# Optimization experiments

Hardware: AMD Instinct MI355X
Metric: run time of the kernel (lower is better)

## Reference

```python
import jax, jax.numpy as jnp
import numpy as np

BN_EPS = 1e-5


def setup_inputs() -> dict:
    key = jax.random.key(0)
    ks = jax.random.split(key, 5)
    b, c, h, w = 4, 128, 64, 64
    x = jax.random.normal(ks[0], (b, c, h, w), dtype=jnp.float32)
    # conv1x1 c -> 2c (fan-in scaled)
    w_inp = jax.random.normal(ks[1], (2 * c, c), dtype=jnp.float32) / np.sqrt(c)
    b_inp = jax.random.normal(ks[2], (2 * c,), dtype=jnp.float32) * 0.01
    bn_gamma = jnp.ones((2 * c,), dtype=jnp.float32)
    bn_beta = jnp.zeros((2 * c,), dtype=jnp.float32)
    bn_mean = jnp.zeros((2 * c,), dtype=jnp.float32)
    bn_var = jnp.ones((2 * c,), dtype=jnp.float32)
    w_out = jax.random.normal(ks[3], (c, c), dtype=jnp.float32) / np.sqrt(c)
    b_out = jax.random.normal(ks[4], (c,), dtype=jnp.float32) * 0.01
    return {
        "x": x, "w_inp": w_inp, "b_inp": b_inp,
        "bn_gamma": bn_gamma, "bn_beta": bn_beta,
        "bn_mean": bn_mean, "bn_var": bn_var,
        "w_out": w_out, "b_out": b_out,
    }


def reference(x, w_inp, b_inp, bn_gamma, bn_beta, bn_mean, bn_var, w_out, b_out):
    b, c, h, w = x.shape
    scale = c ** (-0.5)
    # project_inp: conv1x1 (c -> 2c) + BatchNorm2d (eval mode, running stats)
    t = jnp.einsum('bchw,oc->bohw', x, w_inp) + b_inp[None, :, None, None]
    bn_scale = bn_gamma * jax.lax.rsqrt(bn_var + BN_EPS)
    t = t * bn_scale[None, :, None, None] + (bn_beta - bn_mean * bn_scale)[None, :, None, None]
    # split qv along channels, flatten spatial to tokens: [b, N, c], N = h*w
    q = t[:, :c].reshape(b, c, h * w).transpose(0, 2, 1)
    v = t[:, c:].reshape(b, c, h * w).transpose(0, 2, 1)
    # self-similarity attention on q: [b, N, N]
    atn = jax.nn.softmax(jnp.einsum('bnc,bmc->bnm', q, q) * scale, axis=-1)
    y = jnp.einsum('bnm,bmc->bnc', atn, v)  # [b, N, c]
    y = y.transpose(0, 2, 1).reshape(b, c, h, w)
    # project_out: conv1x1 c -> c
    y = jnp.einsum('bchw,oc->bohw', y, w_out) + b_out[None, :, None, None]
    return (y, atn)
```

## Files before the change

kernel.cpp:

```cpp
#include <hip/hip_runtime.h>
#include <stdint.h>
#include <math.h>

#define C_DIM 128
#define N_TOK 4096
#define NB 4
#define LOG2E 1.4426950408889634f

typedef __attribute__((ext_vector_type(8))) short bf16x8;
typedef __attribute__((ext_vector_type(4))) float f32x4;

__device__ __forceinline__ unsigned short f2bf(float f) {
  unsigned u = __builtin_bit_cast(unsigned, f);
  unsigned r = (u + 0x7FFFu + ((u >> 16) & 1u)) >> 16;
  return (unsigned short)r;
}
__device__ __forceinline__ float bf2f(unsigned short h) {
  return __builtin_bit_cast(float, ((unsigned)h) << 16);
}
__device__ __forceinline__ void gload_lds16(const void* g, void* l) {
  __builtin_amdgcn_global_load_lds((const __attribute__((address_space(1))) void*)g,
                                   (__attribute__((address_space(3))) void*)l,
                                   16, 0, 0);
}

__global__ __launch_bounds__(256) void proj_in_kernel(
    const float* __restrict__ x, const float* __restrict__ w_inp,
    const float* __restrict__ b_inp, const float* __restrict__ gamma,
    const float* __restrict__ beta, const float* __restrict__ mean,
    const float* __restrict__ var,
    unsigned short* __restrict__ q, unsigned short* __restrict__ vT) {
  __shared__ char smem[35840];
  unsigned short* xh = (unsigned short*)smem;
  unsigned short* xl = (unsigned short*)(smem + 17408);

  const int tid = threadIdx.x;
  const int b = blockIdx.x >> 6;
  const int n0 = (blockIdx.x & 63) << 6;
  const int lane = tid & 63;
  const int wave = tid >> 6;
  const int l15 = lane & 15, lg = lane >> 4;

  {
    const int c = tid >> 1;
    const int j0 = (tid & 1) * 32;
    const float* src = x + ((size_t)b * C_DIM + c) * N_TOK + n0 + j0;
#pragma unroll
    for (int j = 0; j < 32; j += 4) {
      float4 v4 = *(const float4*)(src + j);
#pragma unroll
      for (int e = 0; e < 4; e++) {
        float f = (&v4.x)[e];
        unsigned short hi = f2bf(f);
        unsigned short lo = f2bf(f - bf2f(hi));
        int n = j0 + j + e;
        xh[n * 136 + c] = hi;
        xl[n * 136 + c] = lo;
      }
    }
  }
  __syncthreads();

  f32x4 acc[4][4];
#pragma unroll
  for (int i = 0; i < 4; i++)
#pragma unroll
    for (int j = 0; j < 4; j++) acc[i][j] = {0.f, 0.f, 0.f, 0.f};

#pragma unroll
  for (int ks = 0; ks < 4; ks++) {
    bf16x8 ah[4], al[4];
#pragma unroll
    for (int ot = 0; ot < 4; ot++) {
      const int o = wave * 64 + ot * 16 + l15;
      const float* wp = w_inp + o * C_DIM + ks * 32 + lg * 8;
      float4 w0 = *(const float4*)wp;
      float4 w1 = *(const float4*)(wp + 4);
#pragma unroll
      for (int e = 0; e < 8; e++) {
        float f = (e < 4) ? (&w0.x)[e] : (&w1.x)[e - 4];
        unsigned short hi = f2bf(f);
        ah[ot][e] = (short)hi;
        al[ot][e] = (short)f2bf(f - bf2f(hi));
      }
    }
#pragma unroll
    for (int nt = 0; nt < 4; nt++) {
      const int off = (nt * 16 + l15) * 136 + ks * 32 + lg * 8;
      bf16x8 bh = *(const bf16x8*)(xh + off);
      bf16x8 bl = *(const bf16x8*)(xl + off);
#pragma unroll
      for (int ot = 0; ot < 4; ot++) {
        acc[ot][nt] = __builtin_amdgcn_mfma_f32_16x16x32_bf16(ah[ot], bh, acc[ot][nt], 0, 0, 0);
        acc[ot][nt] = __builtin_amdgcn_mfma_f32_16x16x32_bf16(ah[ot], bl, acc[ot][nt], 0, 0, 0);
        acc[ot][nt] = __builtin_amdgcn_mfma_f32_16x16x32_bf16(al[ot], bh, acc[ot][nt], 0, 0, 0);
      }
    }
  }
  __syncthreads();

  unsigned short* qT = (unsigned short*)smem;
  unsigned short* vTl = (unsigned short*)(smem + 17408);

#pragma unroll
  for (int ot = 0; ot < 4; ot++) {
#pragma unroll
    for (int r = 0; r < 4; r++) {
      const int o = wave * 64 + ot * 16 + lg * 4 + r;
      float A = gamma[o] * rsqrtf(var[o] + 1e-5f);
      float Bo = beta[o] + (b_inp[o] - mean[o]) * A;
#pragma unroll
      for (int nt = 0; nt < 4; nt++) {
        float val = acc[ot][nt][r] * A + Bo;
        unsigned short hv = f2bf(val);
        int n = nt * 16 + l15;
        if (wave < 2) {
          qT[n * 136 + o] = hv;
        } else {
          vTl[(o - 128) * 72 + n] = hv;
        }
      }
    }
  }
  __syncthreads();
  {
    int j = tid >> 2, c0 = (tid & 3) * 32;
    unsigned short* dst = q + ((size_t)b * N_TOK + n0 + j) * C_DIM + c0;
    const unsigned short* s = qT + j * 136 + c0;
#pragma unroll
    for (int i = 0; i < 32; i += 8) *(bf16x8*)(dst + i) = *(const bf16x8*)(s + i);
  }
  {
    int c = tid >> 1, h = (tid & 1) * 32;
    unsigned short* dst = vT + ((size_t)b * C_DIM + c) * N_TOK + n0 + h;
    const unsigned short* s = vTl + c * 72 + h;
#pragma unroll
    for (int i = 0; i < 32; i += 8) *(bf16x8*)(dst + i) = *(const bf16x8*)(s + i);
  }
}

__global__ __launch_bounds__(256) void attn_kernel(
    const unsigned short* __restrict__ q, const unsigned short* __restrict__ vT,
    const float* __restrict__ w_out, const float* __restrict__ b_out,
    float* __restrict__ yout, float* __restrict__ atn) {
  __shared__ char smem[71168];

  const int tid = threadIdx.x;
  const int lane = tid & 63;
  const int wave = tid >> 6;
  const int rg = wave >> 1;
  const int kh = wave & 1;
  const int l15 = lane & 15, lg = lane >> 4, l7 = lane & 7;
  const int b = blockIdx.x >> 7;
  const int q0 = (blockIdx.x & 127) << 5;
  const int row0 = q0 + rg * 16;

  const unsigned short* qb = q + (size_t)b * N_TOK * C_DIM;
  const unsigned short* vb = vT + (size_t)b * C_DIM * N_TOK;

  bf16x8 qf[4];
#pragma unroll
  for (int ks = 0; ks < 4; ks++)
    qf[ks] = *(const bf16x8*)(qb + (size_t)(row0 + l15) * C_DIM + ks * 32 + lg * 8);

  int koff[4];
#pragma unroll
  for (int ks = 0; ks < 4; ks++) koff[ks] = (ks * 64 + lg * 16) ^ (l7 * 16);
  const int koff2 = (kh * 64 + lg * 16) ^ (l7 * 16);
  const int krow = l15 * 256;
  const int vrow = l15 * 128;

  auto stageK = [&](int kt, int buf) {
    char* base = smem + buf * 16384;
#pragma unroll
    for (int i = 0; i < 4; i++) {
      int lin = i * 256 + tid;
      int key = lin >> 4;
      int c = ((lin & 15) * 8) ^ ((key & 7) * 8);
      gload_lds16(qb + (size_t)(kt * 64 + key) * C_DIM + c, base + lin * 16);
    }
  };
  auto stageV = [&](int kt, int buf) {
    char* base = smem + 32768 + buf * 16384;
#pragma unroll
    for (int i = 0; i < 4; i++) {
      int lin = i * 256 + tid;
      int c = lin >> 3;
      int key = ((lin & 7) * 8) ^ ((c & 7) * 8);
      gload_lds16(vb + (size_t)c * N_TOK + kt * 64 + key, base + lin * 16);
    }
  };

  const float scale = 0.08838834764831845f;
  float m[4], l[4], invl[4];
#pragma unroll
  for (int r = 0; r < 4; r++) { m[r] = -1e30f; l[r] = 0.f; }

  stageK(0, 0);
  __syncthreads();
  for (int kt = 0; kt < 64; kt++) {
    if (kt + 1 < 64) stageK(kt + 1, (kt + 1) & 1);
    const char* kb = smem + (kt & 1) * 16384;
    float s_all[2][4];
#pragma unroll
    for (int nt16 = 0; nt16 < 2; nt16++) {
      const int nt = kh * 2 + nt16;
      f32x4 acc = {0.f, 0.f, 0.f, 0.f};
#pragma unroll
      for (int ks = 0; ks < 4; ks++) {
        bf16x8 bk = *(const bf16x8*)(kb + nt * 4096 + krow + koff[ks]);
        acc = __builtin_amdgcn_mfma_f32_16x16x32_bf16(qf[ks], bk, acc, 0, 0, 0);
      }
#pragma unroll
      for (int r = 0; r < 4; r++) s_all[nt16][r] = acc[r] * scale;
    }
#pragma unroll
    for (int r = 0; r < 4; r++) {
      float mx = fmaxf(s_all[0][r], s_all[1][r]);
      mx = fmaxf(mx, __shfl_xor(mx, 1));
      mx = fmaxf(mx, __shfl_xor(mx, 2));
      mx = fmaxf(mx, __shfl_xor(mx, 4));
      mx = fmaxf(mx, __shfl_xor(mx, 8));
      float mn = fmaxf(m[r], mx);
      float sum = exp2f((s_all[0][r] - mn) * LOG2E) + exp2f((s_all[1][r] - mn) * LOG2E);
      sum += __shfl_xor(sum, 1);
      sum += __shfl_xor(sum, 2);
      sum += __shfl_xor(sum, 4);
      sum += __shfl_xor(sum, 8);
      l[r] = l[r] * exp2f((m[r] - mn) * LOG2E) + sum;
      m[r] = mn;
    }
    __syncthreads();
  }

  float* statsL = (float*)(smem + 70656);
  if (l15 == 0) {
#pragma unroll
    for (int r = 0; r < 4; r++) {
      float* p = statsL + (((kh * 2 + rg) * 16) + lg * 4 + r) * 2;
      p[0] = m[r];
      p[1] = l[r];
    }
  }
  __syncthreads();
#pragma unroll
  for (int r = 0; r < 4; r++) {
    const int row = lg * 4 + r;
    const float* p0 = statsL + ((rg * 16) + row) * 2;
    const float* p1 = statsL + (((2 + rg) * 16) + row) * 2;
    float m0 = p0[0], l0 = p0[1], m1 = p1[0], l1 = p1[1];
    float M = fmaxf(m0, m1);
    float L = l0 * exp2f((m0 - M) * LOG2E) + l1 * exp2f((m1 - M) * LOG2E);
    m[r] = M;
    invl[r] = 1.0f / L;
  }

  f32x4 yacc[8];
#pragma unroll
  for (int ct = 0; ct < 8; ct++) yacc[ct] = {0.f, 0.f, 0.f, 0.f};

  stageK(0, 0);
  stageV(0, 0);
  __syncthreads();
  unsigned short* pb = (unsigned short*)(smem + 65536 + wave * 1280);
  float* atnb = atn + ((size_t)b * N_TOK + row0) * N_TOK;

  for (int kt = 0; kt < 64; kt++) {
    if (kt + 1 < 64) { stageK(kt + 1, (kt + 1) & 1); stageV(kt + 1, (kt + 1) & 1); }
    const char* kb = smem + (kt & 1) * 16384;
    const char* vbf = smem + 32768 + (kt & 1) * 16384;
#pragma unroll
    for (int nt16 = 0; nt16 < 2; nt16++) {
      const int nt = kh * 2 + nt16;
      f32x4 acc = {0.f, 0.f, 0.f, 0.f};
#pragma unroll
      for (int ks = 0; ks < 4; ks++) {
        bf16x8 bk = *(const bf16x8*)(kb + nt * 4096 + krow + koff[ks]);
        acc = __builtin_amdgcn_mfma_f32_16x16x32_bf16(qf[ks], bk, acc, 0, 0, 0);
      }
#pragma unroll
      for (int r = 0; r < 4; r++) {
        float p = exp2f((acc[r] * scale - m[r]) * LOG2E) * invl[r];
        atnb[(size_t)(lg * 4 + r) * N_TOK + kt * 64 + kh * 32 + nt16 * 16 + l15] = p;
        pb[(lg * 4 + r) * 40 + nt16 * 16 + l15] = (unsigned short)f2bf(p);
      }
    }
    {
      bf16x8 ap = *(const bf16x8*)(pb + l15 * 40 + lg * 8);
#pragma unroll
      for (int ct = 0; ct < 8; ct++) {
        bf16x8 bv = *(const bf16x8*)(vbf + ct * 2048 + vrow + koff2);
        yacc[ct] = __builtin_amdgcn_mfma_f32_16x16x32_bf16(ap, bv, yacc[ct], 0, 0, 0);
      }
    }
    __syncthreads();
  }

  float* ymergeF = (float*)(smem + 32768);
  if (kh) {
#pragma unroll
    for (int ct = 0; ct < 8; ct++)
#pragma unroll
      for (int r = 0; r < 4; r++)
        ymergeF[(rg * 16 + lg * 4 + r) * 136 + ct * 16 + l15] = yacc[ct][r];
  }
  __syncthreads();
  if (!kh) {
#pragma unroll
    for (int ct = 0; ct < 8; ct++)
#pragma unroll
      for (int r = 0; r < 4; r++)
        yacc[ct][r] += ymergeF[(rg * 16 + lg * 4 + r) * 136 + ct * 16 + l15];

    unsigned short* yl = (unsigned short*)(smem + rg * 16384);
    float* ol = (float*)(smem + rg * 16384 + 4608);
#pragma unroll
    for (int ct = 0; ct < 8; ct++)
#pragma unroll
      for (int r = 0; r < 4; r++)
        yl[(lg * 4 + r) * 136 + ct * 16 + l15] = f2bf(yacc[ct][r]);

    bf16x8 af[4];
#pragma unroll
    for (int ks = 0; ks < 4; ks++)
      af[ks] = *(const bf16x8*)(yl + l15 * 136 + ks * 32 + lg * 8);

#pragma unroll
    for (int cot = 0; cot < 8; cot++) {
      f32x4 oacc = {0.f, 0.f, 0.f, 0.f};
#pragma unroll
      for (int ks = 0; ks < 4; ks++) {
        const float* wp = w_out + (cot * 16 + l15) * C_DIM + ks * 32 + lg * 8;
        float4 w0 = *(const float4*)wp;
        float4 w1 = *(const float4*)(wp + 4);
        bf16x8 bw;
#pragma unroll
        for (int e = 0; e < 8; e++) bw[e] = (short)f2bf((e < 4) ? (&w0.x)[e] : (&w1.x)[e - 4]);
        oacc = __builtin_amdgcn_mfma_f32_16x16x32_bf16(af[ks], bw, oacc, 0, 0, 0);
      }
      float bo = b_out[cot * 16 + l15];
#pragma unroll
      for (int r = 0; r < 4; r++) ol[(cot * 16 + l15) * 20 + lg * 4 + r] = oacc[r] + bo;
    }
#pragma unroll
    for (int i = 0; i < 2; i++) {
      int co = i * 64 + lane;
      float* dst = yout + ((size_t)b * C_DIM + co) * N_TOK + row0;
      const float* s = ol + co * 20;
#pragma unroll
      for (int jj = 0; jj < 16; jj += 4) *(float4*)(dst + jj) = *(const float4*)(s + jj);
    }
  }
}

extern "C" void kernel_launch(void* const* d_in, const int* in_sizes, int n_in,
                              void* d_out, int out_size, void* d_ws, size_t ws_size,
                              hipStream_t stream) {
  const float* x = (const float*)d_in[0];
  const float* w_inp = (const float*)d_in[1];
  const float* b_inp = (const float*)d_in[2];
  const float* gamma = (const float*)d_in[3];
  const float* beta = (const float*)d_in[4];
  const float* mean = (const float*)d_in[5];
  const float* var = (const float*)d_in[6];
  const float* w_out = (const float*)d_in[7];
  const float* b_out = (const float*)d_in[8];

  float* out = (float*)d_out;
  float* yout = out;
  float* atn = out + (size_t)NB * C_DIM * N_TOK;

  unsigned short* q = (unsigned short*)d_ws;
  unsigned short* vT = q + (size_t)NB * N_TOK * C_DIM;

  proj_in_kernel<<<256, 256, 0, stream>>>(x, w_inp, b_inp, gamma, beta, mean, var, q, vT);
  attn_kernel<<<512, 256, 0, stream>>>(q, vT, w_out, b_out, yout, atn);
}
```

Measured before the change: 212.8 us.

## Replace online softmax max with global norm bound; fuse PV into first sweep

New measurement: 231.1 us. 8.6% more time.

```diff
diff --git a/kernel.cpp b/kernel.cpp
--- a/kernel.cpp
+++ b/kernel.cpp
@@ -8,6 +8,7 @@
 #define LOG2E 1.4426950408889634f
 
 typedef __attribute__((ext_vector_type(8))) short bf16x8;
+typedef __attribute__((ext_vector_type(4))) short bf16x4;
 typedef __attribute__((ext_vector_type(4))) float f32x4;
 
 __device__ __forceinline__ unsigned short f2bf(float f) {
@@ -29,10 +30,12 @@
     const float* __restrict__ b_inp, const float* __restrict__ gamma,
     const float* __restrict__ beta, const float* __restrict__ mean,
     const float* __restrict__ var,
-    unsigned short* __restrict__ q, unsigned short* __restrict__ vT) {
-  __shared__ char smem[35840];
+    unsigned short* __restrict__ q, unsigned short* __restrict__ vT,
+    int* __restrict__ m2bits) {
+  __shared__ char smem[36096];
   unsigned short* xh = (unsigned short*)smem;
   unsigned short* xl = (unsigned short*)(smem + 17408);
+  float* blkred = (float*)(smem + 35840);
 
   const int tid = threadIdx.x;
   const int b = blockIdx.x >> 6;
@@ -137,13 +140,38 @@
 #pragma unroll
     for (int i = 0; i < 32; i += 8) *(bf16x8*)(dst + i) = *(const bf16x8*)(s + i);
   }
+  {
+    int row = tid >> 2, qn = tid & 3;
+    const unsigned short* qr = qT + row * 136 + qn * 32;
+    float s = 0.f;
+#pragma unroll
+    for (int i = 0; i < 32; i++) {
+      float f = bf2f(qr[i]);
+      s = fmaf(f, f, s);
+    }
+    s += __shfl_xor(s, 1);
+    s += __shfl_xor(s, 2);
+    if ((tid & 3) == 0) blkred[row] = s;
+    __syncthreads();
+    if (tid < 64) {
+      float v = blkred[tid];
+      v = fmaxf(v, __shfl_xor(v, 1));
+      v = fmaxf(v, __shfl_xor(v, 2));
+      v = fmaxf(v, __shfl_xor(v, 4));
+      v = fmaxf(v, __shfl_xor(v, 8));
+      v = fmaxf(v, __shfl_xor(v, 16));
+      v = fmaxf(v, __shfl_xor(v, 32));
+      if (tid == 0) atomicMax(m2bits, __float_as_int(v));
+    }
+  }
 }
 
 __global__ __launch_bounds__(256) void attn_kernel(
     const unsigned short* __restrict__ q, const unsigned short* __restrict__ vT,
     const float* __restrict__ w_out, const float* __restrict__ b_out,
-    float* __restrict__ yout, float* __restrict__ atn) {
-  __shared__ char smem[71168];
+    float* __restrict__ yout, float* __restrict__ atn,
+    const float* __restrict__ m2ptr) {
+  __shared__ char smem[55552];
 
   const int tid = threadIdx.x;
   const int lane = tid & 63;
@@ -158,6 +186,10 @@
   const unsigned short* qb = q + (size_t)b * N_TOK * C_DIM;
   const unsigned short* vb = vT + (size_t)b * C_DIM * N_TOK;
 
+  const float scale = 0.08838834764831845f;
+  const float ke = scale * LOG2E;
+  const float nmk = -(m2ptr[0]) * ke;
+
   bf16x8 qf[4];
 #pragma unroll
   for (int ks = 0; ks < 4; ks++)
@@ -166,9 +198,7 @@
   int koff[4];
 #pragma unroll
   for (int ks = 0; ks < 4; ks++) koff[ks] = (ks * 64 + lg * 16) ^ (l7 * 16);
-  const int koff2 = (kh * 64 + lg * 16) ^ (l7 * 16);
   const int krow = l15 * 256;
-  const int vrow = l15 * 128;
 
   auto stageK = [&](int kt, int buf) {
     char* base = smem + buf * 16384;
@@ -180,123 +210,82 @@
       gload_lds16(qb + (size_t)(kt * 64 + key) * C_DIM + c, base + lin * 16);
     }
   };
-  auto stageV = [&](int kt, int buf) {
-    char* base = smem + 32768 + buf * 16384;
-#pragma unroll
-    for (int i = 0; i < 4; i++) {
-      int lin = i * 256 + tid;
-      int c = lin >> 3;
-      int key = ((lin & 7) * 8) ^ ((c & 7) * 8);
-      gload_lds16(vb + (size_t)c * N_TOK + kt * 64 + key, base + lin * 16);
-    }
+
+  unsigned short* pbuf = (unsigned short*)(smem + 32768 + wave * 1280);
+  float* statsL = (float*)(smem + 37888);
+  float* ymergeF = (float*)(smem + 38144);
+
+  const unsigned short* vlane = vb + (size_t)l15 * N_TOK + kh * 32 + lg * 8;
+
+  float lpart = 0.f;
+  f32x4 yacc[8];
+#pragma unroll
+  for (int ct = 0; ct < 8; ct++) yacc[ct] = {0.f, 0.f, 0.f, 0.f};
+
+  bf16x8 vA[8], vB[8];
+  stageK(0, 0);
+#pragma unroll
+  for (int ct = 0; ct < 8; ct++) vA[ct] = *(const bf16x8*)(vlane + (size_t)ct * 16 * N_TOK);
+  __syncthreads();
+
+  unsigned short* pbw0 = pbuf + l15 * 40 + lg * 4;
+  unsigned short* pbw1 = pbuf + l15 * 40 + 16 + lg * 4;
+  const unsigned short* par = pbuf + l15 * 40 + lg * 8;
+
+  auto sweep1_iter = [&](int kt, bf16x8(&vc)[8], bf16x8(&vn)[8]) {
+    if (kt + 1 < 64) {
+      stageK(kt + 1, (kt + 1) & 1);
+      const unsigned short* vp = vlane + (size_t)(kt + 1) * 64;
+#pragma unroll
+      for (int ct = 0; ct < 8; ct++) vn[ct] = *(const bf16x8*)(vp + (size_t)ct * 16 * N_TOK);
+    }
+    const char* kb = smem + (kt & 1) * 16384;
+#pragma unroll
+    for (int nt = 0; nt < 2; nt++) {
+      f32x4 acc = {0.f, 0.f, 0.f, 0.f};
+#pragma unroll
+      for (int ks = 0; ks < 4; ks++) {
+        bf16x8 ak = *(const bf16x8*)(kb + (kh * 2 + nt) * 4096 + krow + koff[ks]);
+        acc = __builtin_amdgcn_mfma_f32_16x16x32_bf16(ak, qf[ks], acc, 0, 0, 0);
+      }
+      bf16x4 pk;
+#pragma unroll
+      for (int r = 0; r < 4; r++) {
+        float p = __builtin_amdgcn_exp2f(fmaf(acc[r], ke, nmk));
+        lpart += p;
+        pk[r] = (short)f2bf(p);
+      }
+      *(bf16x4*)(nt ? pbw1 : pbw0) = pk;
+    }
+    bf16x8 ap = *(const bf16x8*)par;
+#pragma unroll
+    for (int ct = 0; ct < 8; ct++)
+      yacc[ct] = __builtin_amdgcn_mfma_f32_16x16x32_bf16(ap, vc[ct], yacc[ct], 0, 0, 0);
+    __syncthreads();
   };
 
-  const float scale = 0.08838834764831845f;
-  float m[4], l[4], invl[4];
-#pragma unroll
-  for (int r = 0; r < 4; r++) { m[r] = -1e30f; l[r] = 0.f; }
-
-  stageK(0, 0);
-  __syncthreads();
-  for (int kt = 0; kt < 64; kt++) {
-    if (kt + 1 < 64) stageK(kt + 1, (kt + 1) & 1);
-    const char* kb = smem + (kt & 1) * 16384;
-    float s_all[2][4];
-#pragma unroll
-    for (int nt16 = 0; nt16 < 2; nt16++) {
-      const int nt = kh * 2 + nt16;
-      f32x4 acc = {0.f, 0.f, 0.f, 0.f};
-#pragma unroll
-      for (int ks = 0; ks < 4; ks++) {
-        bf16x8 bk = *(const bf16x8*)(kb + nt * 4096 + krow + koff[ks]);
-        acc = __builtin_amdgcn_mfma_f32_16x16x32_bf16(qf[ks], bk, acc, 0, 0, 0);
-      }
-#pragma unroll
-      for (int r = 0; r < 4; r++) s_all[nt16][r] = acc[r] * scale;
-    }
-#pragma unroll
-    for (int r = 0; r < 4; r++) {
-      float mx = fmaxf(s_all[0][r], s_all[1][r]);
-      mx = fmaxf(mx, __shfl_xor(mx, 1));
-      mx = fmaxf(mx, __shfl_xor(mx, 2));
-      mx = fmaxf(mx, __shfl_xor(mx, 4));
-      mx = fmaxf(mx, __shfl_xor(mx, 8));
-      float mn = fmaxf(m[r], mx);
-      float sum = exp2f((s_all[0][r] - mn) * LOG2E) + exp2f((s_all[1][r] - mn) * LOG2E);
-      sum += __shfl_xor(sum, 1);
-      sum += __shfl_xor(sum, 2);
-      sum += __shfl_xor(sum, 4);
-      sum += __shfl_xor(sum, 8);
-      l[r] = l[r] * exp2f((m[r] - mn) * LOG2E) + sum;
-      m[r] = mn;
-    }
-    __syncthreads();
-  }
-
-  float* statsL = (float*)(smem + 70656);
-  if (l15 == 0) {
-#pragma unroll
-    for (int r = 0; r < 4; r++) {
-      float* p = statsL + (((kh * 2 + rg) * 16) + lg * 4 + r) * 2;
-      p[0] = m[r];
-      p[1] = l[r];
-    }
-  }
-  __syncthreads();
+  for (int kt = 0; kt < 64; kt += 2) {
+    sweep1_iter(kt, vA, vB);
+    sweep1_iter(kt + 1, vB, vA);
+  }
+
+  lpart += __shfl_xor(lpart, 16);
+  lpart += __shfl_xor(lpart, 32);
+  if (lg == 0) statsL[kh * 32 + rg * 16 + l15] = lpart;
+  __syncthreads();
+
+  float invl_r[4];
 #pragma unroll
   for (int r = 0; r < 4; r++) {
-    const int row = lg * 4 + r;
-    const float* p0 = statsL + ((rg * 16) + row) * 2;
-    const float* p1 = statsL + (((2 + rg) * 16) + row) * 2;
-    float m0 = p0[0], l0 = p0[1], m1 = p1[0], l1 = p1[1];
-    float M = fmaxf(m0, m1);
-    float L = l0 * exp2f((m0 - M) * LOG2E) + l1 * exp2f((m1 - M) * LOG2E);
-    m[r] = M;
-    invl[r] = 1.0f / L;
-  }
-
-  f32x4 yacc[8];
-#pragma unroll
-  for (int ct = 0; ct < 8; ct++) yacc[ct] = {0.f, 0.f, 0.f, 0.f};
-
-  stageK(0, 0);
-  stageV(0, 0);
-  __syncthreads();
-  unsigned short* pb = (unsigned short*)(smem + 65536 + wave * 1280);
-  float* atnb = atn + ((size_t)b * N_TOK + row0) * N_TOK;
-
-  for (int kt = 0; kt < 64; kt++) {
-    if (kt + 1 < 64) { stageK(kt + 1, (kt + 1) & 1); stageV(kt + 1, (kt + 1) & 1); }
-    const char* kb = smem + (kt & 1) * 16384;
-    const char* vbf = smem + 32768 + (kt & 1) * 16384;
-#pragma unroll
-    for (int nt16 = 0; nt16 < 2; nt16++) {
-      const int nt = kh * 2 + nt16;
-      f32x4 acc = {0.f, 0.f, 0.f, 0.f};
-#pragma unroll
-      for (int ks = 0; ks < 4; ks++) {
-        bf16x8 bk = *(const bf16x8*)(kb + nt * 4096 + krow + koff[ks]);
-        acc = __builtin_amdgcn_mfma_f32_16x16x32_bf16(qf[ks], bk, acc, 0, 0, 0);
-      }
-#pragma unroll
-      for (int r = 0; r < 4; r++) {
-        float p = exp2f((acc[r] * scale - m[r]) * LOG2E) * invl[r];
-        atnb[(size_t)(lg * 4 + r) * N_TOK + kt * 64 + kh * 32 + nt16 * 16 + l15] = p;
-        pb[(lg * 4 + r) * 40 + nt16 * 16 + l15] = (unsigned short)f2bf(p);
-      }
-    }
-    {
-      bf16x8 ap = *(const bf16x8*)(pb + l15 * 40 + lg * 8);
-#pragma unroll
-      for (int ct = 0; ct < 8; ct++) {
-        bf16x8 bv = *(const bf16x8*)(vbf + ct * 2048 + vrow + koff2);
-        yacc[ct] = __builtin_amdgcn_mfma_f32_16x16x32_bf16(ap, bv, yacc[ct], 0, 0, 0);
-      }
-    }
-    __syncthreads();
-  }
-
-  float* ymergeF = (float*)(smem + 32768);
+    float ls = statsL[rg * 16 + lg * 4 + r] + statsL[32 + rg * 16 + lg * 4 + r];
+    invl_r[r] = 1.0f / ls;
+  }
+  float invl2;
+  {
+    float ls = statsL[rg * 16 + l15] + statsL[32 + rg * 16 + l15];
+    invl2 = 1.0f / ls;
+  }
+
   if (kh) {
 #pragma unroll
     for (int ct = 0; ct < 8; ct++)
@@ -310,7 +299,7 @@
     for (int ct = 0; ct < 8; ct++)
 #pragma unroll
       for (int r = 0; r < 4; r++)
-        yacc[ct][r] += ymergeF[(rg * 16 + lg * 4 + r) * 136 + ct * 16 + l15];
+        yacc[ct][r] = (yacc[ct][r] + ymergeF[(rg * 16 + lg * 4 + r) * 136 + ct * 16 + l15]) * invl_r[r];
 
     unsigned short* yl = (unsigned short*)(smem + rg * 16384);
     float* ol = (float*)(smem + rg * 16384 + 4608);
@@ -350,6 +339,31 @@
 #pragma unroll
       for (int jj = 0; jj < 16; jj += 4) *(float4*)(dst + jj) = *(const float4*)(s + jj);
     }
+  }
+  __syncthreads();
+
+  stageK(0, 0);
+  __syncthreads();
+  float* atnp = atn + ((size_t)b * N_TOK + row0 + l15) * N_TOK + kh * 32 + lg * 4;
+  for (int kt = 0; kt < 64; kt++) {
+    if (kt + 1 < 64) stageK(kt + 1, (kt + 1) & 1);
+    const char* kb = smem + (kt & 1) * 16384;
+#pragma unroll
+    for (int nt = 0; nt < 2; nt++) {
+      f32x4 acc = {0.f, 0.f, 0.f, 0.f};
+#pragma unroll
+      for (int ks = 0; ks < 4; ks++) {
+        bf16x8 ak = *(const bf16x8*)(kb + (kh * 2 + nt) * 4096 + krow + koff[ks]);
+        acc = __builtin_amdgcn_mfma_f32_16x16x32_bf16(ak, qf[ks], acc, 0, 0, 0);
+      }
+      float4 o;
+#pragma unroll
+      for (int r = 0; r < 4; r++)
+        (&o.x)[r] = __builtin_amdgcn_exp2f(fmaf(acc[r], ke, nmk)) * invl2;
+      *(float4*)(atnp + nt * 16) = o;
+    }
+    atnp += 64;
+    __syncthreads();
   }
 }
 
@@ -372,7 +386,9 @@
 
   unsigned short* q = (unsigned short*)d_ws;
   unsigned short* vT = q + (size_t)NB * N_TOK * C_DIM;
-
-  proj_in_kernel<<<256, 256, 0, stream>>>(x, w_inp, b_inp, gamma, beta, mean, var, q, vT);
-  attn_kernel<<<512, 256, 0, stream>>>(q, vT, w_out, b_out, yout, atn);
-}
+  int* m2bits = (int*)(vT + (size_t)NB * C_DIM * N_TOK);
+
+  hipMemsetAsync(m2bits, 0, 4, stream);
+  proj_in_kernel<<<256, 256, 0, stream>>>(x, w_inp, b_inp, gamma, beta, mean, var, q, vT, m2bits);
+  attn_kernel<<<512, 256, 0, stream>>>(q, vT, w_out, b_out, yout, atn, (const float*)m2bits);
+}
```
